# Performance work log

Measured on AMD Instinct MI355X. Metric: run time of the kernel, lower is better.

The kernel has to match this reference:

```python
import jax, jax.numpy as jnp
import numpy as np
import math

B, MSA, L, D = 1, 64, 256, 512
H = 8
DH = D // H  # 64


def setup_inputs() -> dict:
    key = jax.random.key(0)
    ks = jax.random.split(key, 6)
    x = jax.random.normal(ks[0], (B, MSA, L, D), dtype=jnp.float32)
    Wq = jax.random.normal(ks[1], (D, D), dtype=jnp.float32) * (1.0 / math.sqrt(D))
    Wk = jax.random.normal(ks[2], (D, D), dtype=jnp.float32) * (1.0 / math.sqrt(D))
    Wv = jax.random.normal(ks[3], (D, D), dtype=jnp.float32) * (1.0 / math.sqrt(D))
    aK = jax.random.normal(ks[4], (L, L, DH), dtype=jnp.float32)
    aV = jax.random.normal(ks[5], (L, L, DH), dtype=jnp.float32)
    return {"x": x, "Wq": Wq, "Wk": Wk, "Wv": Wv, "aK": aK, "aV": aV}


def _proj(t, W, b, m, l, h, dh):
    # nn.Linear(bias=False): t @ W.T, then split heads -> (B,H,MSA,L,dh)
    y = jnp.einsum('bmld,ed->bmle', t, W).reshape(b, m, l, h, dh)
    return jnp.transpose(y, (0, 3, 1, 2, 4))


def reference(x, Wq, Wk, Wv, aK, aV):
    b, m, l, d = x.shape
    h, dh = H, DH
    q = _proj(x, Wq, b, m, l, h, dh)  # (B,H,MSA,L,dh)
    k = _proj(x, Wk, b, m, l, h, dh)
    v = _proj(x, Wv, b, m, l, h, dh)
    # content score + relative-position score
    e1 = jnp.einsum('bhmid,bhmjd->bhmij', q, k)           # (B,H,MSA,L,L)
    e2 = jnp.einsum('bhmid,ijd->bhmij', q, aK)            # (B,H,MSA,L,L)
    alpha = jax.nn.softmax((e1 + e2) / math.sqrt(dh), axis=-1)
    z1 = jnp.einsum('bhmij,bhmjd->bhmid', alpha, v)       # content output
    z2 = jnp.einsum('bhmij,ijd->bhmid', alpha, aV)        # relative-V output
    z = (z1 + z2).sum(axis=2)                             # sum over MSA -> (B,H,L,dh)
    out = jnp.transpose(z, (0, 2, 1, 3)).reshape(b, l, d) # (B,L,D)
    return out
```

## Files before the change

### kernel.cpp

```cpp
#include <hip/hip_runtime.h>

#define THREADS 256

typedef unsigned short u16;
typedef __attribute__((ext_vector_type(8))) short bf16x8;
typedef __attribute__((ext_vector_type(4))) float f32x4;

__device__ __forceinline__ u16 f2bf(float f) {
  unsigned int u = __float_as_uint(f);
  u += 0x7fffu + ((u >> 16) & 1u);
  return (u16)(u >> 16);
}
__device__ __forceinline__ float bf2f(u16 s) {
  return __uint_as_float(((unsigned int)s) << 16);
}
__device__ __forceinline__ bf16x8 ld8g(const u16* p) {
  return *reinterpret_cast<const bf16x8*>(p);
}
__device__ __forceinline__ bf16x8 ld8s(const u16* p) {
  return *reinterpret_cast<const bf16x8*>(p);
}
__device__ __forceinline__ void st4bf(u16* dst, float4 v) {
  unsigned int lo = (unsigned int)f2bf(v.x) | ((unsigned int)f2bf(v.y) << 16);
  unsigned int hi = (unsigned int)f2bf(v.z) | ((unsigned int)f2bf(v.w) << 16);
  uint2 u; u.x = lo; u.y = hi;
  *reinterpret_cast<uint2*>(dst) = u;
}
__device__ __forceinline__ uint4 pack8(float4 a, float4 b) {
  uint4 r;
  r.x = (unsigned int)f2bf(a.x) | ((unsigned int)f2bf(a.y) << 16);
  r.y = (unsigned int)f2bf(a.z) | ((unsigned int)f2bf(a.w) << 16);
  r.z = (unsigned int)f2bf(b.x) | ((unsigned int)f2bf(b.y) << 16);
  r.w = (unsigned int)f2bf(b.z) | ((unsigned int)f2bf(b.w) << 16);
  return r;
}
typedef __attribute__((address_space(1))) const unsigned int g_u32;
typedef __attribute__((address_space(3))) unsigned int l_u32;
__device__ __forceinline__ void async16(const u16* g, u16* l) {
  __builtin_amdgcn_global_load_lds((g_u32*)g, (l_u32*)l, 16, 0, 0);
}

__global__ __launch_bounds__(THREADS) void cast_xw(
    const float* __restrict__ x, const float* __restrict__ wq,
    const float* __restrict__ wk, const float* __restrict__ wv,
    u16* __restrict__ xb, u16* __restrict__ wqb, u16* __restrict__ wkb,
    u16* __restrict__ wvb) {
  int t = blockIdx.x * THREADS + threadIdx.x;
  if (t < 2097152) {
    st4bf(xb + t * 4, reinterpret_cast<const float4*>(x)[t]);
  } else if (t < 2162688) {
    int q = t - 2097152;
    st4bf(wqb + q * 4, reinterpret_cast<const float4*>(wq)[q]);
  } else if (t < 2228224) {
    int q = t - 2162688;
    st4bf(wkb + q * 4, reinterpret_cast<const float4*>(wk)[q]);
  } else if (t < 2293760) {
    int q = t - 2228224;
    st4bf(wvb + q * 4, reinterpret_cast<const float4*>(wv)[q]);
  }
}

__global__ __launch_bounds__(THREADS) void proj_gemm(
    const u16* __restrict__ xb, const u16* __restrict__ wb,
    u16* __restrict__ qh, u16* __restrict__ kb, u16* __restrict__ vt) {
  const int bm = blockIdx.x / 12, bn = blockIdx.x % 12;
  const int tid = threadIdx.x;
  const int wave = tid >> 6, lane = tid & 63;
  const int quad = lane >> 4, l15 = lane & 15;
  __shared__ __align__(16) u16 smem[9216];
  u16* At = smem;
  u16* Bt = smem + 4096;

  const int rowL = lane >> 2;
  const int chunkL = (lane & 3) ^ ((lane >> 3) & 3);
  const u16* gA = xb + (size_t)(bm * 128 + wave * 32 + rowL) * 512 + chunkL * 8;
  const u16* gB = wb + (size_t)(bn * 128 + wave * 32 + rowL) * 512 + chunkL * 8;
  u16* lA = At + wave * 1024;
  u16* lB = Bt + wave * 1024;

  const int rw0 = (wave & 1) * 64, cw0 = (wave >> 1) * 64;
  const int swz = (quad ^ ((l15 >> 1) & 3)) * 8;

  f32x4 acc[4][4];
#pragma unroll
  for (int mt = 0; mt < 4; ++mt)
#pragma unroll
    for (int nt = 0; nt < 4; ++nt) acc[mt][nt] = (f32x4){0.f, 0.f, 0.f, 0.f};

  for (int s = 0; s < 16; ++s) {
    __syncthreads();
    async16(gA + s * 32, lA);
    async16(gA + s * 32 + 8192, lA + 512);
    async16(gB + s * 32, lB);
    async16(gB + s * 32 + 8192, lB + 512);
    __syncthreads();
    bf16x8 af[4], bf[4];
#pragma unroll
    for (int mt = 0; mt < 4; ++mt)
      af[mt] = ld8s(At + (rw0 + mt * 16 + l15) * 32 + swz);
#pragma unroll
    for (int nt = 0; nt < 4; ++nt)
      bf[nt] = ld8s(Bt + (cw0 + nt * 16 + l15) * 32 + swz);
#pragma unroll
    for (int mt = 0; mt < 4; ++mt)
#pragma unroll
      for (int nt = 0; nt < 4; ++nt)
        acc[mt][nt] = __builtin_amdgcn_mfma_f32_16x16x32_bf16(af[mt], bf[nt], acc[mt][nt], 0, 0, 0);
  }

  const int mat = bn >> 2;
  const int h0 = (bn & 3) * 2;
  const int m = bm >> 1;
  const int l0 = (bm & 1) * 128;

  if (mat < 2) {
    u16* dstb = (mat == 0) ? qh : kb;
    const int il = tid >> 1, cc = (tid & 1) * 32;
#pragma unroll
    for (int p = 0; p < 2; ++p) {
      __syncthreads();
      if ((wave >> 1) == p) {
#pragma unroll
        for (int mt = 0; mt < 4; ++mt)
#pragma unroll
          for (int nt = 0; nt < 4; ++nt)
#pragma unroll
            for (int r = 0; r < 4; ++r)
              smem[(rw0 + mt * 16 + quad * 4 + r) * 72 + nt * 16 + l15] =
                  f2bf(acc[mt][nt][r]);
      }
      __syncthreads();
      u16* dst = dstb + ((size_t)((h0 + p) * 64 + m) * 256 + l0 + il) * 64 + cc;
      uint4 v0 = *reinterpret_cast<uint4*>(&smem[il * 72 + cc]);
      uint4 v1 = *reinterpret_cast<uint4*>(&smem[il * 72 + cc + 8]);
      uint4 v2 = *reinterpret_cast<uint4*>(&smem[il * 72 + cc + 16]);
      uint4 v3 = *reinterpret_cast<uint4*>(&smem[il * 72 + cc + 24]);
      *reinterpret_cast<uint4*>(dst) = v0;
      *reinterpret_cast<uint4*>(dst + 8) = v1;
      *reinterpret_cast<uint4*>(dst + 16) = v2;
      *reinterpret_cast<uint4*>(dst + 24) = v3;
    }
  } else {
    const int tl = tid >> 2, cc = (tid & 3) * 32;
#pragma unroll
    for (int p = 0; p < 2; ++p) {
      __syncthreads();
      if ((wave >> 1) == p) {
#pragma unroll
        for (int mt = 0; mt < 4; ++mt)
#pragma unroll
          for (int nt = 0; nt < 4; ++nt)
#pragma unroll
            for (int r = 0; r < 4; ++r)
              smem[(nt * 16 + l15) * 136 + rw0 + mt * 16 + quad * 4 + r] =
                  f2bf(acc[mt][nt][r]);
      }
      __syncthreads();
      int hm = (h0 + p) * 64 + m;
      u16* dst = vt + (size_t)hm * 16384 + tl * 256 + l0 + cc;
      uint4 v0 = *reinterpret_cast<uint4*>(&smem[tl * 136 + cc]);
      uint4 v1 = *reinterpret_cast<uint4*>(&smem[tl * 136 + cc + 8]);
      uint4 v2 = *reinterpret_cast<uint4*>(&smem[tl * 136 + cc + 16]);
      uint4 v3 = *reinterpret_cast<uint4*>(&smem[tl * 136 + cc + 24]);
      *reinterpret_cast<uint4*>(dst) = v0;
      *reinterpret_cast<uint4*>(dst + 8) = v1;
      *reinterpret_cast<uint4*>(dst + 16) = v2;
      *reinterpret_cast<uint4*>(dst + 24) = v3;
    }
  }
}

__global__ __launch_bounds__(THREADS) void e2_k(
    const u16* __restrict__ qh, const float* __restrict__ aK,
    u16* __restrict__ e2g) {
  const int i = blockIdx.x >> 3, hmt = blockIdx.x & 7;
  const int tid = threadIdx.x;
  const int wave = tid >> 6, lane = tid & 63;
  const int quad = lane >> 4, l15 = lane & 15;
  __shared__ u16 aKl[256 * 72];
#pragma unroll
  for (int c = 0; c < 8; ++c) {
    int fidx = c * 2048 + tid * 8;
    int j = fidx >> 6, d = fidx & 63;
    float4 f0 = *reinterpret_cast<const float4*>(aK + i * 16384 + fidx);
    float4 f1 = *reinterpret_cast<const float4*>(aK + i * 16384 + fidx + 4);
    *reinterpret_cast<uint4*>(&aKl[j * 72 + d]) = pack8(f0, f1);
  }
  __syncthreads();
  f32x4 acc[16];
#pragma unroll
  for (int nt = 0; nt < 16; ++nt) acc[nt] = (f32x4){0.f, 0.f, 0.f, 0.f};
  bf16x8 a[2];
#pragma unroll
  for (int ks = 0; ks < 2; ++ks)
    a[ks] = ld8g(qh + ((hmt * 64 + wave * 16 + l15) * 256 + i) * 64 + ks * 32 + quad * 8);
#pragma unroll
  for (int nt = 0; nt < 16; ++nt) {
#pragma unroll
    for (int ks = 0; ks < 2; ++ks) {
      bf16x8 b = ld8s(&aKl[(nt * 16 + l15) * 72 + ks * 32 + quad * 8]);
      acc[nt] = __builtin_amdgcn_mfma_f32_16x16x32_bf16(a[ks], b, acc[nt], 0, 0, 0);
    }
  }
  __syncthreads();
  u16* S = aKl;
#pragma unroll
  for (int nt = 0; nt < 16; ++nt)
#pragma unroll
    for (int r = 0; r < 4; ++r)
      S[(wave * 16 + quad * 4 + r) * 264 + nt * 16 + l15] = f2bf(acc[nt][r]);
  __syncthreads();
#pragma unroll
  for (int c = 0; c < 8; ++c) {
    int lin = c * 2048 + tid * 8;
    int row = lin >> 8, col = lin & 255;
    uint4 v = *reinterpret_cast<uint4*>(&S[row * 264 + col]);
    *reinterpret_cast<uint4*>(e2g + ((size_t)(hmt * 64 + row) * 256 + i) * 256 + col) = v;
  }
}

__global__ __launch_bounds__(THREADS) void attn_k(
    const u16* __restrict__ qh, const u16* __restrict__ kb,
    const u16* __restrict__ vt, u16* __restrict__ e2g,
    u16* __restrict__ z1p) {
  const int bi = blockIdx.x;
  const int hm = bi & 511, it = bi >> 9;
  const int tid = threadIdx.x;
  const int wave = tid >> 6, lane = tid & 63;
  const int quad = lane >> 4, l15 = lane & 15;
  __shared__ u16 As[4 * 4224];
  u16* W = &As[wave * 4224];
#pragma unroll
  for (int c = 0; c < 8; ++c) {
    int lin = c * 512 + lane * 8;
    int row = lin >> 8, col = lin & 255;
    uint4 v = *reinterpret_cast<const uint4*>(
        e2g + ((size_t)hm * 256 + it * 64 + wave * 16 + row) * 256 + col);
    *reinterpret_cast<uint4*>(&W[row * 264 + col]) = v;
  }
  __syncthreads();
  f32x4 acc[16];
#pragma unroll
  for (int nt = 0; nt < 16; ++nt) acc[nt] = (f32x4){0.f, 0.f, 0.f, 0.f};
  bf16x8 a[2];
#pragma unroll
  for (int ks = 0; ks < 2; ++ks)
    a[ks] = ld8g(qh + ((size_t)hm * 256 + it * 64 + wave * 16 + l15) * 64 + ks * 32 + quad * 8);
#pragma unroll
  for (int nt = 0; nt < 16; ++nt) {
#pragma unroll
    for (int ks = 0; ks < 2; ++ks) {
      bf16x8 b = ld8g(kb + ((size_t)hm * 256 + nt * 16 + l15) * 64 + ks * 32 + quad * 8);
      acc[nt] = __builtin_amdgcn_mfma_f32_16x16x32_bf16(a[ks], b, acc[nt], 0, 0, 0);
    }
  }
#pragma unroll
  for (int nt = 0; nt < 16; ++nt) {
#pragma unroll
    for (int r = 0; r < 4; ++r) {
      float e2v = bf2f(W[(quad * 4 + r) * 264 + nt * 16 + l15]);
      acc[nt][r] = (acc[nt][r] + e2v) * 0.125f;
    }
  }
#pragma unroll
  for (int r = 0; r < 4; ++r) {
    float mx = -3.0e38f;
#pragma unroll
    for (int nt = 0; nt < 16; ++nt) mx = fmaxf(mx, acc[nt][r]);
    for (int msk = 1; msk < 16; msk <<= 1) mx = fmaxf(mx, __shfl_xor(mx, msk));
    float s = 0.f;
#pragma unroll
    for (int nt = 0; nt < 16; ++nt) {
      float p = expf(acc[nt][r] - mx);
      acc[nt][r] = p;
      s += p;
    }
    for (int msk = 1; msk < 16; msk <<= 1) s += __shfl_xor(s, msk);
    float inv = 1.0f / s;
    int lrow = quad * 4 + r;
#pragma unroll
    for (int nt = 0; nt < 16; ++nt)
      W[lrow * 264 + nt * 16 + l15] = f2bf(acc[nt][r] * inv);
  }
  __syncthreads();
#pragma unroll
  for (int c = 0; c < 8; ++c) {
    int lin = c * 512 + lane * 8;
    int row = lin >> 8, col = lin & 255;
    uint4 v = *reinterpret_cast<uint4*>(&W[row * 264 + col]);
    *reinterpret_cast<uint4*>(
        e2g + ((size_t)hm * 256 + it * 64 + wave * 16 + row) * 256 + col) = v;
  }
  f32x4 acc2[4];
#pragma unroll
  for (int nt = 0; nt < 4; ++nt) acc2[nt] = (f32x4){0.f, 0.f, 0.f, 0.f};
#pragma unroll
  for (int ks = 0; ks < 8; ++ks) {
    bf16x8 a2 = ld8s(&W[l15 * 264 + ks * 32 + quad * 8]);
#pragma unroll
    for (int nt = 0; nt < 4; ++nt) {
      bf16x8 b2 = ld8g(vt + (size_t)hm * 16384 + (nt * 16 + l15) * 256 + ks * 32 + quad * 8);
      acc2[nt] = __builtin_amdgcn_mfma_f32_16x16x32_bf16(a2, b2, acc2[nt], 0, 0, 0);
    }
  }
  __syncthreads();
#pragma unroll
  for (int nt = 0; nt < 4; ++nt)
#pragma unroll
    for (int r = 0; r < 4; ++r)
      W[(quad * 4 + r) * 264 + nt * 16 + l15] = f2bf(acc2[nt][r]);
  __syncthreads();
  {
    int row = lane >> 2, col = (lane & 3) * 16;
    uint4 v0 = *reinterpret_cast<uint4*>(&W[row * 264 + col]);
    uint4 v1 = *reinterpret_cast<uint4*>(&W[row * 264 + col + 8]);
    u16* dst = z1p + (size_t)hm * 16384 + (it * 64 + wave * 16 + row) * 64 + col;
    *reinterpret_cast<uint4*>(dst) = v0;
    *reinterpret_cast<uint4*>(dst + 8) = v1;
  }
}

__global__ __launch_bounds__(THREADS) void beta_k(
    const u16* __restrict__ alphag, float* __restrict__ beta) {
  const int b = blockIdx.x;
  const int h = b >> 8, i = b & 255;
  const int j = threadIdx.x;
  float s = 0.f;
  const u16* base = alphag + (size_t)(h * 64) * 65536 + i * 256 + j;
#pragma unroll 4
  for (int m = 0; m < 64; ++m) s += bf2f(base[(size_t)m * 65536]);
  beta[(h * 256 + i) * 256 + j] = s;
}

__global__ __launch_bounds__(THREADS) void z2_k(
    const float* __restrict__ beta, const float* __restrict__ aV,
    float* __restrict__ z2b) {
  const int i = blockIdx.x;
  const int tid = threadIdx.x;
  const int wave = tid >> 6, lane = tid & 63;
  const int quad = lane >> 4, l15 = lane & 15;
  __shared__ u16 aVl[64 * 264];
#pragma unroll
  for (int c = 0; c < 8; ++c) {
    int fidx = c * 2048 + tid * 8;
    int j = fidx >> 6, d = fidx & 63;
    float4 f0 = *reinterpret_cast<const float4*>(aV + (size_t)i * 16384 + fidx);
    float4 f1 = *reinterpret_cast<const float4*>(aV + (size_t)i * 16384 + fidx + 4);
    float fv[8] = {f0.x, f0.y, f0.z, f0.w, f1.x, f1.y, f1.z, f1.w};
#pragma unroll
    for (int u = 0; u < 8; ++u) aVl[(d + u) * 264 + j] = f2bf(fv[u]);
  }
  __syncthreads();
  f32x4 acc = (f32x4){0.f, 0.f, 0.f, 0.f};
#pragma unroll
  for (int ks = 0; ks < 8; ++ks) {
    u16 ab[8];
    if (l15 < 8) {
      const float* bp = beta + (l15 * 256 + i) * 256 + ks * 32 + quad * 8;
      float4 f0 = *reinterpret_cast<const float4*>(bp);
      float4 f1 = *reinterpret_cast<const float4*>(bp + 4);
      ab[0] = f2bf(f0.x); ab[1] = f2bf(f0.y); ab[2] = f2bf(f0.z); ab[3] = f2bf(f0.w);
      ab[4] = f2bf(f1.x); ab[5] = f2bf(f1.y); ab[6] = f2bf(f1.z); ab[7] = f2bf(f1.w);
    } else {
#pragma unroll
      for (int u = 0; u < 8; ++u) ab[u] = 0;
    }
    bf16x8 a = *reinterpret_cast<bf16x8*>(ab);
    bf16x8 b = ld8s(&aVl[(wave * 16 + l15) * 264 + ks * 32 + quad * 8]);
    acc = __builtin_amdgcn_mfma_f32_16x16x32_bf16(a, b, acc, 0, 0, 0);
  }
#pragma unroll
  for (int r = 0; r < 4; ++r) {
    int h = quad * 4 + r;
    if (h < 8) z2b[i * 512 + h * 64 + wave * 16 + l15] = acc[r];
  }
}

__global__ __launch_bounds__(THREADS) void reduce_k(
    const u16* __restrict__ z1p, const float* __restrict__ z2b,
    float* __restrict__ out) {
  int o = blockIdx.x * THREADS + threadIdx.x;
  int i = o >> 9, e = o & 511;
  int h = e >> 6, d = e & 63;
  float s = z2b[o];
  const u16* base = z1p + (size_t)(h * 64) * 16384 + i * 64 + d;
#pragma unroll 4
  for (int m = 0; m < 64; ++m) s += bf2f(base[(size_t)m * 16384]);
  out[o] = s;
}

extern "C" void kernel_launch(void* const* d_in, const int* in_sizes, int n_in,
                              void* d_out, int out_size, void* d_ws, size_t ws_size,
                              hipStream_t stream) {
  const float* x  = (const float*)d_in[0];
  const float* wq = (const float*)d_in[1];
  const float* wk = (const float*)d_in[2];
  const float* wv = (const float*)d_in[3];
  const float* aK = (const float*)d_in[4];
  const float* aV = (const float*)d_in[5];
  float* out = (float*)d_out;

  char* ws = (char*)d_ws;
  u16* xb    = (u16*)(ws + 0);
  u16* wqb   = (u16*)(ws + 16777216);
  u16* wkb   = (u16*)(ws + 17301504);
  u16* wvb   = (u16*)(ws + 17825792);
  float* beta= (float*)(ws + 18350080);
  float* z2b = (float*)(ws + 20447232);
  u16* qh    = (u16*)(ws + 35127296);
  u16* kb    = (u16*)(ws + 51904512);
  u16* vt    = (u16*)(ws + 68681728);
  u16* e2g   = (u16*)(ws + 85458944);
  u16* z1p   = xb;

  cast_xw<<<8960, THREADS, 0, stream>>>(x, wq, wk, wv, xb, wqb, wkb, wvb);
  proj_gemm<<<1536, THREADS, 0, stream>>>(xb, wqb, qh, kb, vt);
  e2_k<<<2048, THREADS, 0, stream>>>(qh, aK, e2g);
  attn_k<<<2048, THREADS, 0, stream>>>(qh, kb, vt, e2g, z1p);
  beta_k<<<2048, THREADS, 0, stream>>>(e2g, beta);
  z2_k<<<256, THREADS, 0, stream>>>(beta, aV, z2b);
  reduce_k<<<512, THREADS, 0, stream>>>(z1p, z2b, out);
}
```

Baseline: 299.4 us.

## Fuse per-MSA alpha summation into attention kernel, processing four MSA rows per block

The attention kernel now loops over four MSA slices per block and accumulates softmax probabilities and z1 outputs in registers. It writes one partial beta and one partial z1 per group of four instead of the full alpha tensor and per-MSA z1. This removes the alpha write-back and shrinks the beta and final reductions from 64 terms to 16, cutting global memory traffic. In exchange the grid shrinks to 512 blocks, register pressure rises from the extra accumulators, and e2 is now read straight from global memory without staging in LDS.

```diff
diff --git a/kernel.cpp b/kernel.cpp
--- a/kernel.cpp
+++ b/kernel.cpp
@@ -219,117 +219,130 @@
   }
 }
 
-__global__ __launch_bounds__(THREADS) void attn_k(
+__global__ __launch_bounds__(THREADS, 2) void attn_f(
     const u16* __restrict__ qh, const u16* __restrict__ kb,
-    const u16* __restrict__ vt, u16* __restrict__ e2g,
-    u16* __restrict__ z1p) {
+    const u16* __restrict__ vt, const u16* __restrict__ e2g,
+    u16* __restrict__ betap, u16* __restrict__ z1q) {
   const int bi = blockIdx.x;
-  const int hm = bi & 511, it = bi >> 9;
+  const int it = bi >> 7;
+  const int hmc = bi & 127;
+  const int h = hmc >> 4, mc = hmc & 15;
   const int tid = threadIdx.x;
   const int wave = tid >> 6, lane = tid & 63;
   const int quad = lane >> 4, l15 = lane & 15;
   __shared__ u16 As[4 * 4224];
   u16* W = &As[wave * 4224];
-#pragma unroll
-  for (int c = 0; c < 8; ++c) {
-    int lin = c * 512 + lane * 8;
-    int row = lin >> 8, col = lin & 255;
-    uint4 v = *reinterpret_cast<const uint4*>(
-        e2g + ((size_t)hm * 256 + it * 64 + wave * 16 + row) * 256 + col);
-    *reinterpret_cast<uint4*>(&W[row * 264 + col]) = v;
-  }
-  __syncthreads();
-  f32x4 acc[16];
-#pragma unroll
-  for (int nt = 0; nt < 16; ++nt) acc[nt] = (f32x4){0.f, 0.f, 0.f, 0.f};
-  bf16x8 a[2];
-#pragma unroll
-  for (int ks = 0; ks < 2; ++ks)
-    a[ks] = ld8g(qh + ((size_t)hm * 256 + it * 64 + wave * 16 + l15) * 64 + ks * 32 + quad * 8);
-#pragma unroll
-  for (int nt = 0; nt < 16; ++nt) {
-#pragma unroll
-    for (int ks = 0; ks < 2; ++ks) {
-      bf16x8 b = ld8g(kb + ((size_t)hm * 256 + nt * 16 + l15) * 64 + ks * 32 + quad * 8);
-      acc[nt] = __builtin_amdgcn_mfma_f32_16x16x32_bf16(a[ks], b, acc[nt], 0, 0, 0);
-    }
-  }
-#pragma unroll
-  for (int nt = 0; nt < 16; ++nt) {
+  const int i0 = it * 64 + wave * 16;
+
+  f32x4 betaacc[16];
+  f32x4 acc2[4];
+#pragma unroll
+  for (int nt = 0; nt < 16; ++nt) betaacc[nt] = (f32x4){0.f, 0.f, 0.f, 0.f};
+#pragma unroll
+  for (int nt = 0; nt < 4; ++nt) acc2[nt] = (f32x4){0.f, 0.f, 0.f, 0.f};
+
+  for (int mi = 0; mi < 4; ++mi) {
+    const int hm = h * 64 + mc * 4 + mi;
+    f32x4 acc[16];
+    const u16* e2p = e2g + ((size_t)hm * 256 + i0 + quad * 4) * 256 + l15;
+#pragma unroll
+    for (int nt = 0; nt < 16; ++nt)
+#pragma unroll
+      for (int r = 0; r < 4; ++r)
+        acc[nt][r] = bf2f(e2p[r * 256 + nt * 16]);
+    bf16x8 a[2];
+#pragma unroll
+    for (int ks = 0; ks < 2; ++ks)
+      a[ks] = ld8g(qh + ((size_t)hm * 256 + i0 + l15) * 64 + ks * 32 + quad * 8);
+#pragma unroll
+    for (int nt = 0; nt < 16; ++nt) {
+#pragma unroll
+      for (int ks = 0; ks < 2; ++ks) {
+        bf16x8 b = ld8g(kb + ((size_t)hm * 256 + nt * 16 + l15) * 64 + ks * 32 + quad * 8);
+        acc[nt] = __builtin_amdgcn_mfma_f32_16x16x32_bf16(a[ks], b, acc[nt], 0, 0, 0);
+      }
+    }
 #pragma unroll
     for (int r = 0; r < 4; ++r) {
-      float e2v = bf2f(W[(quad * 4 + r) * 264 + nt * 16 + l15]);
-      acc[nt][r] = (acc[nt][r] + e2v) * 0.125f;
-    }
-  }
-#pragma unroll
-  for (int r = 0; r < 4; ++r) {
-    float mx = -3.0e38f;
-#pragma unroll
-    for (int nt = 0; nt < 16; ++nt) mx = fmaxf(mx, acc[nt][r]);
-    for (int msk = 1; msk < 16; msk <<= 1) mx = fmaxf(mx, __shfl_xor(mx, msk));
-    float s = 0.f;
-#pragma unroll
-    for (int nt = 0; nt < 16; ++nt) {
-      float p = expf(acc[nt][r] - mx);
-      acc[nt][r] = p;
-      s += p;
-    }
-    for (int msk = 1; msk < 16; msk <<= 1) s += __shfl_xor(s, msk);
-    float inv = 1.0f / s;
-    int lrow = quad * 4 + r;
-#pragma unroll
-    for (int nt = 0; nt < 16; ++nt)
-      W[lrow * 264 + nt * 16 + l15] = f2bf(acc[nt][r] * inv);
-  }
-  __syncthreads();
+      float mx = -3.0e38f;
+#pragma unroll
+      for (int nt = 0; nt < 16; ++nt) mx = fmaxf(mx, acc[nt][r]);
+      for (int msk = 1; msk < 16; msk <<= 1) mx = fmaxf(mx, __shfl_xor(mx, msk));
+      float s = 0.f;
+#pragma unroll
+      for (int nt = 0; nt < 16; ++nt) {
+        float p = expf((acc[nt][r] - mx) * 0.125f);
+        acc[nt][r] = p;
+        s += p;
+      }
+      for (int msk = 1; msk < 16; msk <<= 1) s += __shfl_xor(s, msk);
+      float inv = 1.0f / s;
+      int lrow = quad * 4 + r;
+#pragma unroll
+      for (int nt = 0; nt < 16; ++nt) {
+        float av = acc[nt][r] * inv;
+        betaacc[nt][r] += av;
+        W[lrow * 264 + nt * 16 + l15] = f2bf(av);
+      }
+    }
+#pragma unroll
+    for (int ks = 0; ks < 8; ++ks) {
+      bf16x8 a2 = ld8s(&W[l15 * 264 + ks * 32 + quad * 8]);
+#pragma unroll
+      for (int nt = 0; nt < 4; ++nt) {
+        bf16x8 b2 = ld8g(vt + (size_t)hm * 16384 + (nt * 16 + l15) * 256 + ks * 32 + quad * 8);
+        acc2[nt] = __builtin_amdgcn_mfma_f32_16x16x32_bf16(a2, b2, acc2[nt], 0, 0, 0);
+      }
+    }
+  }
+
+#pragma unroll
+  for (int nt = 0; nt < 16; ++nt)
+#pragma unroll
+    for (int r = 0; r < 4; ++r)
+      W[(quad * 4 + r) * 264 + nt * 16 + l15] = f2bf(betaacc[nt][r]);
 #pragma unroll
   for (int c = 0; c < 8; ++c) {
     int lin = c * 512 + lane * 8;
     int row = lin >> 8, col = lin & 255;
     uint4 v = *reinterpret_cast<uint4*>(&W[row * 264 + col]);
     *reinterpret_cast<uint4*>(
-        e2g + ((size_t)hm * 256 + it * 64 + wave * 16 + row) * 256 + col) = v;
-  }
-  f32x4 acc2[4];
-#pragma unroll
-  for (int nt = 0; nt < 4; ++nt) acc2[nt] = (f32x4){0.f, 0.f, 0.f, 0.f};
-#pragma unroll
-  for (int ks = 0; ks < 8; ++ks) {
-    bf16x8 a2 = ld8s(&W[l15 * 264 + ks * 32 + quad * 8]);
-#pragma unroll
-    for (int nt = 0; nt < 4; ++nt) {
-      bf16x8 b2 = ld8g(vt + (size_t)hm * 16384 + (nt * 16 + l15) * 256 + ks * 32 + quad * 8);
-      acc2[nt] = __builtin_amdgcn_mfma_f32_16x16x32_bf16(a2, b2, acc2[nt], 0, 0, 0);
-    }
-  }
-  __syncthreads();
+        betap + ((size_t)hmc * 256 + it * 64 + wave * 16 + row) * 256 + col) = v;
+  }
 #pragma unroll
   for (int nt = 0; nt < 4; ++nt)
 #pragma unroll
     for (int r = 0; r < 4; ++r)
-      W[(quad * 4 + r) * 264 + nt * 16 + l15] = f2bf(acc2[nt][r]);
-  __syncthreads();
+      W[(quad * 4 + r) * 72 + nt * 16 + l15] = f2bf(acc2[nt][r]);
   {
     int row = lane >> 2, col = (lane & 3) * 16;
-    uint4 v0 = *reinterpret_cast<uint4*>(&W[row * 264 + col]);
-    uint4 v1 = *reinterpret_cast<uint4*>(&W[row * 264 + col + 8]);
-    u16* dst = z1p + (size_t)hm * 16384 + (it * 64 + wave * 16 + row) * 64 + col;
+    uint4 v0 = *reinterpret_cast<uint4*>(&W[row * 72 + col]);
+    uint4 v1 = *reinterpret_cast<uint4*>(&W[row * 72 + col + 8]);
+    u16* dst = z1q + ((size_t)hmc * 256 + it * 64 + wave * 16 + row) * 64 + col;
     *reinterpret_cast<uint4*>(dst) = v0;
     *reinterpret_cast<uint4*>(dst + 8) = v1;
   }
 }
 
-__global__ __launch_bounds__(THREADS) void beta_k(
-    const u16* __restrict__ alphag, float* __restrict__ beta) {
-  const int b = blockIdx.x;
-  const int h = b >> 8, i = b & 255;
-  const int j = threadIdx.x;
-  float s = 0.f;
-  const u16* base = alphag + (size_t)(h * 64) * 65536 + i * 256 + j;
-#pragma unroll 4
-  for (int m = 0; m < 64; ++m) s += bf2f(base[(size_t)m * 65536]);
-  beta[(h * 256 + i) * 256 + j] = s;
+__global__ __launch_bounds__(THREADS) void beta_r(
+    const u16* __restrict__ betap, float* __restrict__ beta) {
+  int t = blockIdx.x * THREADS + threadIdx.x;
+  int hi = t >> 5;
+  int j0 = (t & 31) * 8;
+  int h = hi >> 8, i = hi & 255;
+  const u16* src = betap + ((size_t)(h * 16) * 256 + i) * 256 + j0;
+  float s[8] = {0.f, 0.f, 0.f, 0.f, 0.f, 0.f, 0.f, 0.f};
+#pragma unroll
+  for (int m = 0; m < 16; ++m) {
+    uint4 v = *reinterpret_cast<const uint4*>(src + (size_t)m * 65536);
+    const u16* pv = reinterpret_cast<const u16*>(&v);
+#pragma unroll
+    for (int u = 0; u < 8; ++u) s[u] += bf2f(pv[u]);
+  }
+  float4 o0 = {s[0], s[1], s[2], s[3]};
+  float4 o1 = {s[4], s[5], s[6], s[7]};
+  *reinterpret_cast<float4*>(beta + (size_t)hi * 256 + j0) = o0;
+  *reinterpret_cast<float4*>(beta + (size_t)hi * 256 + j0 + 4) = o1;
 }
 
 __global__ __launch_bounds__(THREADS) void z2_k(
@@ -371,21 +384,21 @@
   }
 #pragma unroll
   for (int r = 0; r < 4; ++r) {
-    int h = quad * 4 + r;
-    if (h < 8) z2b[i * 512 + h * 64 + wave * 16 + l15] = acc[r];
-  }
-}
-
-__global__ __launch_bounds__(THREADS) void reduce_k(
-    const u16* __restrict__ z1p, const float* __restrict__ z2b,
+    int hh = quad * 4 + r;
+    if (hh < 8) z2b[i * 512 + hh * 64 + wave * 16 + l15] = acc[r];
+  }
+}
+
+__global__ __launch_bounds__(THREADS) void final_k(
+    const u16* __restrict__ z1q, const float* __restrict__ z2b,
     float* __restrict__ out) {
   int o = blockIdx.x * THREADS + threadIdx.x;
   int i = o >> 9, e = o & 511;
   int h = e >> 6, d = e & 63;
   float s = z2b[o];
-  const u16* base = z1p + (size_t)(h * 64) * 16384 + i * 64 + d;
-#pragma unroll 4
-  for (int m = 0; m < 64; ++m) s += bf2f(base[(size_t)m * 16384]);
+  const u16* base = z1q + ((size_t)(h * 16) * 256 + i) * 64 + d;
+#pragma unroll
+  for (int m = 0; m < 16; ++m) s += bf2f(base[(size_t)m * 16384]);
   out[o] = s;
 }
 
@@ -405,19 +418,20 @@
   u16* wqb   = (u16*)(ws + 16777216);
   u16* wkb   = (u16*)(ws + 17301504);
   u16* wvb   = (u16*)(ws + 17825792);
-  float* beta= (float*)(ws + 18350080);
-  float* z2b = (float*)(ws + 20447232);
+  u16* betap = (u16*)(ws + 18350080);
   u16* qh    = (u16*)(ws + 35127296);
   u16* kb    = (u16*)(ws + 51904512);
   u16* vt    = (u16*)(ws + 68681728);
   u16* e2g   = (u16*)(ws + 85458944);
-  u16* z1p   = xb;
+  u16* z1q   = xb;
+  float* beta= (float*)(ws + 4194304);
+  float* z2b = (float*)(ws + 6291456);
 
   cast_xw<<<8960, THREADS, 0, stream>>>(x, wq, wk, wv, xb, wqb, wkb, wvb);
   proj_gemm<<<1536, THREADS, 0, stream>>>(xb, wqb, qh, kb, vt);
   e2_k<<<2048, THREADS, 0, stream>>>(qh, aK, e2g);
-  attn_k<<<2048, THREADS, 0, stream>>>(qh, kb, vt, e2g, z1p);
-  beta_k<<<2048, THREADS, 0, stream>>>(e2g, beta);
+  attn_f<<<512, THREADS, 0, stream>>>(qh, kb, vt, e2g, betap, z1q);
+  beta_r<<<256, THREADS, 0, stream>>>(betap, beta);
   z2_k<<<256, THREADS, 0, stream>>>(beta, aV, z2b);
-  reduce_k<<<512, THREADS, 0, stream>>>(z1p, z2b, out);
-}
+  final_k<<<512, THREADS, 0, stream>>>(z1q, z2b, out);
+}
```

Result: faster. 283.5 us (-5.3%).
